# Kernel tuning notes

Hardware: AMD Instinct MI355X
Metric: run time of the kernel (lower is better)

## Reference

```python
import jax, jax.numpy as jnp
import numpy as np

D_MODEL = 1024
N_HEADS = 16
D_HEAD = D_MODEL // N_HEADS
LN_EPS = 1e-5


def setup_inputs() -> dict:
    key = jax.random.key(0)
    ks = jax.random.split(key, 10)
    B, N = 2, 2048
    s = 1.0 / np.sqrt(D_MODEL)
    return {
        "x": jax.random.normal(ks[0], (B, N, D_MODEL), dtype=jnp.float32),
        "Wq": jax.random.normal(ks[1], (D_MODEL, D_MODEL), dtype=jnp.float32) * s,
        "bq": jnp.zeros((D_MODEL,), dtype=jnp.float32),
        "Wk": jax.random.normal(ks[2], (D_MODEL, D_MODEL), dtype=jnp.float32) * s,
        "bk": jnp.zeros((D_MODEL,), dtype=jnp.float32),
        "Wv": jax.random.normal(ks[3], (D_MODEL, D_MODEL), dtype=jnp.float32) * s,
        "bv": jnp.zeros((D_MODEL,), dtype=jnp.float32),
        "Wo": jax.random.normal(ks[4], (D_MODEL, D_MODEL), dtype=jnp.float32) * s,
        "bo": jnp.zeros((D_MODEL,), dtype=jnp.float32),
        "ln_gamma": jnp.ones((D_MODEL,), dtype=jnp.float32),
        "ln_beta": jnp.zeros((D_MODEL,), dtype=jnp.float32),
    }


def reference(x, Wq, bq, Wk, bk, Wv, bv, Wo, bo, ln_gamma, ln_beta):
    B, N, _ = x.shape
    # QKV projections -> [B, H, N, dh]
    def proj(W, b):
        return (x @ W.T + b).reshape(B, N, N_HEADS, D_HEAD).transpose(0, 2, 1, 3)
    Q, K, V = proj(Wq, bq), proj(Wk, bk), proj(Wv, bv)
    # scaled scores [B, H, N, N] with causal mask (is_mask=True)
    scores = jnp.einsum("bhqd,bhkd->bhqk", Q, K) / np.sqrt(D_HEAD)
    causal = jnp.tril(jnp.ones((N, N), dtype=bool))
    scores = jnp.where(causal, scores, -jnp.inf)
    attn = jax.nn.softmax(scores, axis=-1)  # dropout p=0 (eval)
    ctx = jnp.einsum("bhqk,bhkd->bhqd", attn, V)  # [B, H, N, dh]
    ctx = ctx.transpose(0, 2, 1, 3).reshape(B, N, D_MODEL)
    out = ctx @ Wo.T + bo + x  # output proj + residual
    # LayerNorm over last dim
    mu = out.mean(-1, keepdims=True)
    var = out.var(-1, keepdims=True)
    return (out - mu) / jnp.sqrt(var + LN_EPS) * ln_gamma + ln_beta
```

## Files before the change

### kernel.cpp

```cpp
#include <hip/hip_runtime.h>
#include <type_traits>

#define D_MODEL 1024
#define NHEADS 16
#define DHEAD 64
#define SEQ 2048
#define BATCH 2
#define MROWS (BATCH*SEQ)
#define NQT (SEQ/64)

typedef unsigned short ushort_t;
using bf16x8 = __attribute__((ext_vector_type(8))) __bf16;
using us4    = __attribute__((ext_vector_type(4))) unsigned short;
using us8    = __attribute__((ext_vector_type(8))) unsigned short;
using f32x4  = __attribute__((ext_vector_type(4))) float;

__device__ __forceinline__ ushort_t f2bf(float f) {
    unsigned int u = __builtin_bit_cast(unsigned int, f);
    u += 0x7FFFu + ((u >> 16) & 1u);
    return (ushort_t)(u >> 16);
}

__device__ __forceinline__ void gl2lds(const ushort_t* g, ushort_t* l) {
    __builtin_amdgcn_global_load_lds(
        (const __attribute__((address_space(1))) unsigned int*)g,
        (__attribute__((address_space(3))) unsigned int*)l,
        16, 0, 0);
}

__global__ __launch_bounds__(256) void cvt_kernel(
    const float* __restrict__ x,
    const float* __restrict__ wq, const float* __restrict__ wk,
    const float* __restrict__ wv, const float* __restrict__ wo,
    ushort_t* __restrict__ xb,
    ushort_t* __restrict__ wqb, ushort_t* __restrict__ wkb,
    ushort_t* __restrict__ wvb, ushort_t* __restrict__ wob)
{
    const size_t XN = (size_t)MROWS * D_MODEL;
    const size_t WN = (size_t)D_MODEL * D_MODEL;
    size_t i = ((size_t)blockIdx.x * 256 + threadIdx.x) * 4;
    const float* s; ushort_t* d; size_t off;
    if (i < XN) { s = x; d = xb; off = i; }
    else {
        size_t j = i - XN;
        int w = (int)(j / WN);
        off = j - (size_t)w * WN;
        s = (w == 0) ? wq : (w == 1) ? wk : (w == 2) ? wv : wo;
        d = (w == 0) ? wqb : (w == 1) ? wkb : (w == 2) ? wvb : wob;
    }
    const f32x4 v = *(const f32x4*)(s + off);
    us4 o;
    #pragma unroll
    for (int t = 0; t < 4; ++t) o[t] = f2bf(v[t]);
    *(us4*)(d + off) = o;
}

template<typename OutT, bool RES>
__global__ __launch_bounds__(256, 3) void gemm_nt(
    const ushort_t* __restrict__ A,
    const ushort_t* __restrict__ W0, const ushort_t* __restrict__ W1, const ushort_t* __restrict__ W2,
    const float* __restrict__ b0, const float* __restrict__ b1, const float* __restrict__ b2,
    const float* __restrict__ res,
    OutT* __restrict__ Y0, OutT* __restrict__ Y1, OutT* __restrict__ Y2)
{
    constexpr int K = D_MODEL;
    __shared__ ushort_t As[2][128 * 32];
    __shared__ ushort_t Ws[2][128 * 32];

    const int z = blockIdx.z;
    const ushort_t* W  = (z == 0) ? W0 : (z == 1) ? W1 : W2;
    const float* bias  = (z == 0) ? b0 : (z == 1) ? b1 : b2;
    OutT* Y            = (z == 0) ? Y0 : (z == 1) ? Y1 : Y2;

    const int i0 = blockIdx.x * 128;
    const int j0 = blockIdx.y * 128;
    const int tid  = threadIdx.x;
    const int lane = tid & 63;
    const int w    = tid >> 6;
    const int wm   = (w >> 1) * 64;
    const int wn   = (w & 1) * 64;
    const int l15  = lane & 15;
    const int quad = lane >> 4;

    const int srow = lane >> 2;
    const int scol = (lane & 3) * 8;
    const int c0 = w * 2, c1 = w * 2 + 1;
    const ushort_t* gA0 = A + (size_t)(i0 + c0 * 16 + srow) * K + scol;
    const ushort_t* gA1 = A + (size_t)(i0 + c1 * 16 + srow) * K + scol;
    const ushort_t* gW0 = W + (size_t)(j0 + c0 * 16 + srow) * K + scol;
    const ushort_t* gW1 = W + (size_t)(j0 + c1 * 16 + srow) * K + scol;

    f32x4 acc[4][4] = {};

    for (int k0 = 0; k0 < K; k0 += 64) {
        gl2lds(gA0 + k0,      &As[0][c0 * 512]);
        gl2lds(gA1 + k0,      &As[0][c1 * 512]);
        gl2lds(gA0 + k0 + 32, &As[1][c0 * 512]);
        gl2lds(gA1 + k0 + 32, &As[1][c1 * 512]);
        gl2lds(gW0 + k0,      &Ws[0][c0 * 512]);
        gl2lds(gW1 + k0,      &Ws[0][c1 * 512]);
        gl2lds(gW0 + k0 + 32, &Ws[1][c0 * 512]);
        gl2lds(gW1 + k0 + 32, &Ws[1][c1 * 512]);
        __syncthreads();

        #pragma unroll
        for (int s = 0; s < 2; ++s) {
            bf16x8 af[4], wf[4];
            #pragma unroll
            for (int m = 0; m < 4; ++m)
                af[m] = *(const bf16x8*)&As[s][(wm + m * 16 + l15) * 32 + quad * 8];
            #pragma unroll
            for (int n = 0; n < 4; ++n)
                wf[n] = *(const bf16x8*)&Ws[s][(wn + n * 16 + l15) * 32 + quad * 8];
            #pragma unroll
            for (int m = 0; m < 4; ++m)
                #pragma unroll
                for (int n = 0; n < 4; ++n)
                    acc[m][n] = __builtin_amdgcn_mfma_f32_16x16x32_bf16(wf[n], af[m], acc[m][n], 0, 0, 0);
        }
        __syncthreads();
    }

    #pragma unroll
    for (int n = 0; n < 4; ++n) {
        const int col = j0 + wn + n * 16 + quad * 4;
        const f32x4 bv = *(const f32x4*)&bias[col];
        #pragma unroll
        for (int m = 0; m < 4; ++m) {
            const int row = i0 + wm + m * 16 + l15;
            if constexpr (std::is_same<OutT, float>::value) {
                f32x4 v;
                #pragma unroll
                for (int r = 0; r < 4; ++r) v[r] = acc[m][n][r] + bv[r];
                if constexpr (RES) {
                    const f32x4 rv = *(const f32x4*)&res[(size_t)row * D_MODEL + col];
                    #pragma unroll
                    for (int r = 0; r < 4; ++r) v[r] += rv[r];
                }
                *(f32x4*)&Y[(size_t)row * D_MODEL + col] = v;
            } else {
                us4 pk;
                #pragma unroll
                for (int r = 0; r < 4; ++r) pk[r] = f2bf(acc[m][n][r] + bv[r]);
                *(us4*)&Y[(size_t)row * D_MODEL + col] = pk;
            }
        }
    }
}

#define VP 72

__global__ __launch_bounds__(256, 3) void attn_kernel(
    const ushort_t* __restrict__ Qg, const ushort_t* __restrict__ Kg,
    const ushort_t* __restrict__ Vg, ushort_t* __restrict__ Og)
{
    __shared__ ushort_t Kt[2][64 * VP];
    __shared__ ushort_t Vt[2][64 * VP];
    __shared__ ushort_t Pw[64 * VP];
    __shared__ ushort_t OnesR[16 * VP];

    const int bh = blockIdx.y;
    const int b = bh >> 4;
    const int h = bh & 15;
    const int p = blockIdx.x;
    const int tid  = threadIdx.x;
    const int lane = tid & 63;
    const int w    = tid >> 6;
    const int l15  = lane & 15;
    const int quad = lane >> 4;

    const size_t headoff = (size_t)h * DHEAD;
    const ushort_t* Kbase = Kg + (size_t)(b * SEQ) * D_MODEL + headoff;
    const ushort_t* Vbase = Vg + (size_t)(b * SEQ) * D_MODEL + headoff;

    const int krow = tid >> 3;
    const int kb   = tid & 7;
    const int vkey = tid & 63;
    const int dc0  = tid >> 6;
    const int dc1  = dc0 + 4;

    for (int i = tid; i < 16 * VP; i += 256) OnesR[i] = 0x3F80;

    bf16x8 onesf[2];
    bool onesLoaded = false;

    for (int half = 0; half < 2; ++half) {
        const int qt = half ? p : (NQT - 1 - p);
        const int q0 = qt * 64;
        const int qg = q0 + w * 16 + l15;
        const int nkt = qt + 1;

        const size_t qrow = (size_t)(b * SEQ + qg) * D_MODEL + headoff;
        const bf16x8 qf0 = *(const bf16x8*)&Qg[qrow + quad * 8];
        const bf16x8 qf1 = *(const bf16x8*)&Qg[qrow + 32 + quad * 8];

        float m_run = -1e30f;
        f32x4 o[4] = {};
        f32x4 o4 = {};

        us8 kp0, kp1, vp0, vp1;
        kp0 = *(const us8*)&Kbase[(size_t)krow * D_MODEL + kb * 8];
        kp1 = *(const us8*)&Kbase[(size_t)(32 + krow) * D_MODEL + kb * 8];
        vp0 = *(const us8*)&Vbase[(size_t)vkey * D_MODEL + dc0 * 8];
        vp1 = *(const us8*)&Vbase[(size_t)vkey * D_MODEL + dc1 * 8];
        *(us8*)&Kt[0][krow * VP + kb * 8]        = kp0;
        *(us8*)&Kt[0][(32 + krow) * VP + kb * 8] = kp1;
        #pragma unroll
        for (int j = 0; j < 8; ++j) {
            Vt[0][(dc0 * 8 + j) * VP + vkey] = vp0[j];
            Vt[0][(dc1 * 8 + j) * VP + vkey] = vp1[j];
        }
        __syncthreads();

        if (!onesLoaded) {
            onesf[0] = *(const bf16x8*)&OnesR[l15 * VP + quad * 8];
            onesf[1] = *(const bf16x8*)&OnesR[l15 * VP + 32 + quad * 8];
            onesLoaded = true;
        }

        for (int kt = 0; kt < nkt; ++kt) {
            const int cur = kt & 1;
            const int nxt = cur ^ 1;
            const bool pre = (kt + 1 < nkt);
            if (pre) {
                const size_t koff = (size_t)((kt + 1) * 64) * D_MODEL;
                kp0 = *(const us8*)&Kbase[koff + (size_t)krow * D_MODEL + kb * 8];
                kp1 = *(const us8*)&Kbase[koff + (size_t)(32 + krow) * D_MODEL + kb * 8];
                vp0 = *(const us8*)&Vbase[koff + (size_t)vkey * D_MODEL + dc0 * 8];
                vp1 = *(const us8*)&Vbase[koff + (size_t)vkey * D_MODEL + dc1 * 8];
            }

            f32x4 sv[4];
            #pragma unroll
            for (int f = 0; f < 4; ++f) {
                const bf16x8 kf0 = *(const bf16x8*)&Kt[cur][(f * 16 + l15) * VP + quad * 8];
                const bf16x8 kf1 = *(const bf16x8*)&Kt[cur][(f * 16 + l15) * VP + 32 + quad * 8];
                f32x4 s = {};
                s = __builtin_amdgcn_mfma_f32_16x16x32_bf16(kf0, qf0, s, 0, 0, 0);
                s = __builtin_amdgcn_mfma_f32_16x16x32_bf16(kf1, qf1, s, 0, 0, 0);
                sv[f] = s;
            }

            if (kt * 64 + 63 <= q0 + w * 16) {
                #pragma unroll
                for (int f = 0; f < 4; ++f)
                    #pragma unroll
                    for (int r = 0; r < 4; ++r) sv[f][r] *= 0.125f;
            } else {
                #pragma unroll
                for (int f = 0; f < 4; ++f) {
                    #pragma unroll
                    for (int r = 0; r < 4; ++r) {
                        const int kg = kt * 64 + f * 16 + quad * 4 + r;
                        sv[f][r] = (kg <= qg) ? sv[f][r] * 0.125f : -1e30f;
                    }
                }
            }

            float mf[4];
            #pragma unroll
            for (int f = 0; f < 4; ++f)
                mf[f] = fmaxf(fmaxf(sv[f][0], sv[f][1]), fmaxf(sv[f][2], sv[f][3]));
            float mx = fmaxf(fmaxf(mf[0], mf[1]), fmaxf(mf[2], mf[3]));
            mx = fmaxf(mx, __shfl_xor(mx, 16));
            mx = fmaxf(mx, __shfl_xor(mx, 32));
            const float mn = fmaxf(m_run, mx);
            const float al = __expf(m_run - mn);
            m_run = mn;
            #pragma unroll
            for (int f = 0; f < 4; ++f)
                #pragma unroll
                for (int r = 0; r < 4; ++r) sv[f][r] = __expf(sv[f][r] - mn);

            #pragma unroll
            for (int t = 0; t < 4; ++t)
                #pragma unroll
                for (int r = 0; r < 4; ++r) o[t][r] *= al;
            #pragma unroll
            for (int r = 0; r < 4; ++r) o4[r] *= al;

            #pragma unroll
            for (int f = 0; f < 4; ++f) {
                us4 pk;
                #pragma unroll
                for (int r = 0; r < 4; ++r) pk[r] = f2bf(sv[f][r]);
                *(us4*)&Pw[(w * 16 + l15) * VP + f * 16 + quad * 4] = pk;
            }
            __asm__ volatile("s_waitcnt lgkmcnt(0)" ::: "memory");

            #pragma unroll
            for (int s = 0; s < 2; ++s) {
                const bf16x8 pf = *(const bf16x8*)&Pw[(w * 16 + l15) * VP + s * 32 + quad * 8];
                #pragma unroll
                for (int t = 0; t < 4; ++t) {
                    const bf16x8 vf = *(const bf16x8*)&Vt[cur][(t * 16 + l15) * VP + s * 32 + quad * 8];
                    o[t] = __builtin_amdgcn_mfma_f32_16x16x32_bf16(vf, pf, o[t], 0, 0, 0);
                }
                o4 = __builtin_amdgcn_mfma_f32_16x16x32_bf16(onesf[s], pf, o4, 0, 0, 0);
            }

            if (pre) {
                *(us8*)&Kt[nxt][krow * VP + kb * 8]        = kp0;
                *(us8*)&Kt[nxt][(32 + krow) * VP + kb * 8] = kp1;
                #pragma unroll
                for (int j = 0; j < 8; ++j) {
                    Vt[nxt][(dc0 * 8 + j) * VP + vkey] = vp0[j];
                    Vt[nxt][(dc1 * 8 + j) * VP + vkey] = vp1[j];
                }
            }
            __asm__ volatile("s_waitcnt lgkmcnt(0)\n\ts_barrier" ::: "memory");
        }

        const float inv = 1.f / o4[0];
        const size_t orow = (size_t)(b * SEQ + q0 + w * 16 + l15) * D_MODEL + headoff;
        #pragma unroll
        for (int t = 0; t < 4; ++t) {
            us4 pk;
            #pragma unroll
            for (int r = 0; r < 4; ++r) pk[r] = f2bf(o[t][r] * inv);
            *(us4*)&Og[orow + t * 16 + quad * 4] = pk;
        }
    }
}

__global__ __launch_bounds__(256) void ln_kernel(
    const float* __restrict__ X, const float* __restrict__ g,
    const float* __restrict__ bta, float* __restrict__ out)
{
    __shared__ float r1[4], r2[4];
    const int row = blockIdx.x;
    const int tid = threadIdx.x;
    const float* p = X + (size_t)row * D_MODEL;
    float v[4]; float s1 = 0.f, s2 = 0.f;
    #pragma unroll
    for (int i = 0; i < 4; ++i) { v[i] = p[tid + 256 * i]; s1 += v[i]; s2 += v[i] * v[i]; }
    #pragma unroll
    for (int d = 32; d >= 1; d >>= 1) { s1 += __shfl_xor(s1, d); s2 += __shfl_xor(s2, d); }
    if ((tid & 63) == 0) { r1[tid >> 6] = s1; r2[tid >> 6] = s2; }
    __syncthreads();
    s1 = r1[0] + r1[1] + r1[2] + r1[3];
    s2 = r2[0] + r2[1] + r2[2] + r2[3];
    const float mu  = s1 * (1.f / D_MODEL);
    const float var = s2 * (1.f / D_MODEL) - mu * mu;
    const float rstd = rsqrtf(var + 1e-5f);
    #pragma unroll
    for (int i = 0; i < 4; ++i) {
        const int c = tid + 256 * i;
        out[(size_t)row * D_MODEL + c] = (v[i] - mu) * rstd * g[c] + bta[c];
    }
}

extern "C" void kernel_launch(void* const* d_in, const int* in_sizes, int n_in,
                              void* d_out, int out_size, void* d_ws, size_t ws_size,
                              hipStream_t stream) {
    const float* x     = (const float*)d_in[0];
    const float* Wq    = (const float*)d_in[1];
    const float* bq    = (const float*)d_in[2];
    const float* Wk    = (const float*)d_in[3];
    const float* bk    = (const float*)d_in[4];
    const float* Wv    = (const float*)d_in[5];
    const float* bv    = (const float*)d_in[6];
    const float* Wo    = (const float*)d_in[7];
    const float* bo    = (const float*)d_in[8];
    const float* gamma = (const float*)d_in[9];
    const float* beta  = (const float*)d_in[10];

    const size_t XN = (size_t)MROWS * D_MODEL;
    const size_t WN = (size_t)D_MODEL * D_MODEL;
    ushort_t* wsp = (ushort_t*)d_ws;
    ushort_t* xb  = wsp;
    ushort_t* Yq  = wsp + XN;
    ushort_t* Yk  = wsp + 2 * XN;
    ushort_t* Yv  = wsp + 3 * XN;
    ushort_t* Wqb = wsp + 4 * XN;
    ushort_t* Wkb = Wqb + WN;
    ushort_t* Wvb = Wkb + WN;
    ushort_t* Wob = Wvb + WN;
    ushort_t* ctx = xb;
    float*    pre = (float*)d_out;

    cvt_kernel<<<dim3(8192), 256, 0, stream>>>(x, Wq, Wk, Wv, Wo, xb, Wqb, Wkb, Wvb, Wob);

    gemm_nt<ushort_t, false><<<dim3(MROWS / 128, D_MODEL / 128, 3), 256, 0, stream>>>(
        xb, Wqb, Wkb, Wvb, bq, bk, bv, nullptr, Yq, Yk, Yv);

    attn_kernel<<<dim3(SEQ / 128, BATCH * NHEADS), 256, 0, stream>>>(Yq, Yk, Yv, ctx);

    gemm_nt<float, true><<<dim3(MROWS / 128, D_MODEL / 128, 1), 256, 0, stream>>>(
        ctx, Wob, Wob, Wob, bo, bo, bo, x, pre, pre, pre);

    ln_kernel<<<dim3(MROWS), 256, 0, stream>>>(pre, gamma, beta, (float*)d_out);
}
```

Before: 217.2 us.

## Restructure attention: fold softmax scale into Q, exp2, lazy rescale, swizzled LDS

Folds 1/sqrt(dh)*log2(e) into the Q projection epilogue so attention can use exp2 without per-score scaling. Masking now applies only on the diagonal tile, and rescaling of the accumulators is skipped unless the running max grows by more than a threshold. LDS padding is replaced with XOR swizzling, which frees the ones buffer and lets occupancy rise to 4 blocks. The grid now launches one query tile per block, heaviest first, instead of pairing tiles, and MFMA sections get raised wave priority. Native bf16 conversions replace the manual rounding helper. Lazy rescaling carries a numeric risk if the threshold bound is exceeded, and the unpaired grid gives up the built-in load balancing.

```diff
diff --git a/kernel.cpp b/kernel.cpp
--- a/kernel.cpp
+++ b/kernel.cpp
@@ -11,14 +11,19 @@
 
 typedef unsigned short ushort_t;
 using bf16x8 = __attribute__((ext_vector_type(8))) __bf16;
+using bf16x4 = __attribute__((ext_vector_type(4))) __bf16;
 using us4    = __attribute__((ext_vector_type(4))) unsigned short;
 using us8    = __attribute__((ext_vector_type(8))) unsigned short;
 using f32x4  = __attribute__((ext_vector_type(4))) float;
 
-__device__ __forceinline__ ushort_t f2bf(float f) {
-    unsigned int u = __builtin_bit_cast(unsigned int, f);
-    u += 0x7FFFu + ((u >> 16) & 1u);
-    return (ushort_t)(u >> 16);
+#define QSCALE 0.18033688011112042f
+
+__device__ __forceinline__ float fast_exp2(float x) {
+#if __has_builtin(__builtin_amdgcn_exp2f)
+    return __builtin_amdgcn_exp2f(x);
+#else
+    return __expf(x * 0.6931471805599453f);
+#endif
 }
 
 __device__ __forceinline__ void gl2lds(const ushort_t* g, ushort_t* l) {
@@ -49,10 +54,10 @@
         d = (w == 0) ? wqb : (w == 1) ? wkb : (w == 2) ? wvb : wob;
     }
     const f32x4 v = *(const f32x4*)(s + off);
-    us4 o;
-    #pragma unroll
-    for (int t = 0; t < 4; ++t) o[t] = f2bf(v[t]);
-    *(us4*)(d + off) = o;
+    bf16x4 o;
+    #pragma unroll
+    for (int t = 0; t < 4; ++t) o[t] = (__bf16)v[t];
+    *(bf16x4*)(d + off) = o;
 }
 
 template<typename OutT, bool RES>
@@ -61,7 +66,8 @@
     const ushort_t* __restrict__ W0, const ushort_t* __restrict__ W1, const ushort_t* __restrict__ W2,
     const float* __restrict__ b0, const float* __restrict__ b1, const float* __restrict__ b2,
     const float* __restrict__ res,
-    OutT* __restrict__ Y0, OutT* __restrict__ Y1, OutT* __restrict__ Y2)
+    OutT* __restrict__ Y0, OutT* __restrict__ Y1, OutT* __restrict__ Y2,
+    float qsc)
 {
     constexpr int K = D_MODEL;
     __shared__ ushort_t As[2][128 * 32];
@@ -71,6 +77,7 @@
     const ushort_t* W  = (z == 0) ? W0 : (z == 1) ? W1 : W2;
     const float* bias  = (z == 0) ? b0 : (z == 1) ? b1 : b2;
     OutT* Y            = (z == 0) ? Y0 : (z == 1) ? Y1 : Y2;
+    const float sc     = (z == 0) ? qsc : 1.0f;
 
     const int i0 = blockIdx.x * 128;
     const int j0 = blockIdx.y * 128;
@@ -139,30 +146,36 @@
                 }
                 *(f32x4*)&Y[(size_t)row * D_MODEL + col] = v;
             } else {
-                us4 pk;
+                bf16x4 pk;
                 #pragma unroll
-                for (int r = 0; r < 4; ++r) pk[r] = f2bf(acc[m][n][r] + bv[r]);
-                *(us4*)&Y[(size_t)row * D_MODEL + col] = pk;
+                for (int r = 0; r < 4; ++r) pk[r] = (__bf16)((acc[m][n][r] + bv[r]) * sc);
+                *(bf16x4*)&Y[(size_t)row * D_MODEL + col] = pk;
             }
         }
     }
 }
 
-#define VP 72
-
-__global__ __launch_bounds__(256, 3) void attn_kernel(
+#define KD 64
+
+__device__ __forceinline__ int kswz(int row, int col) {
+    return row * KD + (col ^ ((row & 7) << 3));
+}
+
+__global__ __launch_bounds__(256, 4) void attn_kernel(
     const ushort_t* __restrict__ Qg, const ushort_t* __restrict__ Kg,
     const ushort_t* __restrict__ Vg, ushort_t* __restrict__ Og)
 {
-    __shared__ ushort_t Kt[2][64 * VP];
-    __shared__ ushort_t Vt[2][64 * VP];
-    __shared__ ushort_t Pw[64 * VP];
-    __shared__ ushort_t OnesR[16 * VP];
-
-    const int bh = blockIdx.y;
+    __shared__ __align__(16) ushort_t Kt[2][64 * KD];
+    __shared__ __align__(16) ushort_t Vt[2][64 * KD];
+    __shared__ __align__(16) ushort_t Pw[64 * KD];
+
+    const int bh = blockIdx.x;
     const int b = bh >> 4;
     const int h = bh & 15;
-    const int p = blockIdx.x;
+    const int qt = (NQT - 1) - blockIdx.y;
+    const int q0 = qt * 64;
+    const int nkt = qt + 1;
+
     const int tid  = threadIdx.x;
     const int lane = tid & 63;
     const int w    = tid >> 6;
@@ -179,147 +192,141 @@
     const int dc0  = tid >> 6;
     const int dc1  = dc0 + 4;
 
-    for (int i = tid; i < 16 * VP; i += 256) OnesR[i] = 0x3F80;
-
-    bf16x8 onesf[2];
-    bool onesLoaded = false;
-
-    for (int half = 0; half < 2; ++half) {
-        const int qt = half ? p : (NQT - 1 - p);
-        const int q0 = qt * 64;
-        const int qg = q0 + w * 16 + l15;
-        const int nkt = qt + 1;
-
-        const size_t qrow = (size_t)(b * SEQ + qg) * D_MODEL + headoff;
-        const bf16x8 qf0 = *(const bf16x8*)&Qg[qrow + quad * 8];
-        const bf16x8 qf1 = *(const bf16x8*)&Qg[qrow + 32 + quad * 8];
-
-        float m_run = -1e30f;
-        f32x4 o[4] = {};
-        f32x4 o4 = {};
-
-        us8 kp0, kp1, vp0, vp1;
-        kp0 = *(const us8*)&Kbase[(size_t)krow * D_MODEL + kb * 8];
-        kp1 = *(const us8*)&Kbase[(size_t)(32 + krow) * D_MODEL + kb * 8];
-        vp0 = *(const us8*)&Vbase[(size_t)vkey * D_MODEL + dc0 * 8];
-        vp1 = *(const us8*)&Vbase[(size_t)vkey * D_MODEL + dc1 * 8];
-        *(us8*)&Kt[0][krow * VP + kb * 8]        = kp0;
-        *(us8*)&Kt[0][(32 + krow) * VP + kb * 8] = kp1;
-        #pragma unroll
-        for (int j = 0; j < 8; ++j) {
-            Vt[0][(dc0 * 8 + j) * VP + vkey] = vp0[j];
-            Vt[0][(dc1 * 8 + j) * VP + vkey] = vp1[j];
-        }
-        __syncthreads();
-
-        if (!onesLoaded) {
-            onesf[0] = *(const bf16x8*)&OnesR[l15 * VP + quad * 8];
-            onesf[1] = *(const bf16x8*)&OnesR[l15 * VP + 32 + quad * 8];
-            onesLoaded = true;
-        }
-
-        for (int kt = 0; kt < nkt; ++kt) {
-            const int cur = kt & 1;
-            const int nxt = cur ^ 1;
-            const bool pre = (kt + 1 < nkt);
-            if (pre) {
-                const size_t koff = (size_t)((kt + 1) * 64) * D_MODEL;
-                kp0 = *(const us8*)&Kbase[koff + (size_t)krow * D_MODEL + kb * 8];
-                kp1 = *(const us8*)&Kbase[koff + (size_t)(32 + krow) * D_MODEL + kb * 8];
-                vp0 = *(const us8*)&Vbase[koff + (size_t)vkey * D_MODEL + dc0 * 8];
-                vp1 = *(const us8*)&Vbase[koff + (size_t)vkey * D_MODEL + dc1 * 8];
-            }
-
-            f32x4 sv[4];
-            #pragma unroll
-            for (int f = 0; f < 4; ++f) {
-                const bf16x8 kf0 = *(const bf16x8*)&Kt[cur][(f * 16 + l15) * VP + quad * 8];
-                const bf16x8 kf1 = *(const bf16x8*)&Kt[cur][(f * 16 + l15) * VP + 32 + quad * 8];
-                f32x4 s = {};
-                s = __builtin_amdgcn_mfma_f32_16x16x32_bf16(kf0, qf0, s, 0, 0, 0);
-                s = __builtin_amdgcn_mfma_f32_16x16x32_bf16(kf1, qf1, s, 0, 0, 0);
-                sv[f] = s;
-            }
-
-            if (kt * 64 + 63 <= q0 + w * 16) {
-                #pragma unroll
-                for (int f = 0; f < 4; ++f)
-                    #pragma unroll
-                    for (int r = 0; r < 4; ++r) sv[f][r] *= 0.125f;
-            } else {
-                #pragma unroll
-                for (int f = 0; f < 4; ++f) {
-                    #pragma unroll
-                    for (int r = 0; r < 4; ++r) {
-                        const int kg = kt * 64 + f * 16 + quad * 4 + r;
-                        sv[f][r] = (kg <= qg) ? sv[f][r] * 0.125f : -1e30f;
-                    }
-                }
-            }
-
-            float mf[4];
-            #pragma unroll
-            for (int f = 0; f < 4; ++f)
-                mf[f] = fmaxf(fmaxf(sv[f][0], sv[f][1]), fmaxf(sv[f][2], sv[f][3]));
-            float mx = fmaxf(fmaxf(mf[0], mf[1]), fmaxf(mf[2], mf[3]));
-            mx = fmaxf(mx, __shfl_xor(mx, 16));
-            mx = fmaxf(mx, __shfl_xor(mx, 32));
-            const float mn = fmaxf(m_run, mx);
-            const float al = __expf(m_run - mn);
-            m_run = mn;
+    const int rx = (l15 & 7) << 3;
+    const int cs0 = (quad * 8) ^ rx;
+    const int cs1 = (32 + quad * 8) ^ rx;
+    int pwc[4];
+    #pragma unroll
+    for (int f = 0; f < 4; ++f) pwc[f] = (f * 16 + quad * 4) ^ rx;
+    ushort_t* PwRow = &Pw[(w * 16 + l15) * KD];
+
+    const int kwa = krow * KD + ((kb * 8) ^ ((krow & 7) << 3));
+
+    const int qg = q0 + w * 16 + l15;
+    const size_t qrow = (size_t)(b * SEQ + qg) * D_MODEL + headoff;
+    const bf16x8 qf0 = *(const bf16x8*)&Qg[qrow + quad * 8];
+    const bf16x8 qf1 = *(const bf16x8*)&Qg[qrow + 32 + quad * 8];
+
+    bf16x8 onesf;
+    #pragma unroll
+    for (int j = 0; j < 8; ++j) onesf[j] = (__bf16)1.0f;
+
+    float m_run = -1e30f;
+    f32x4 o[4] = {};
+    f32x4 o4 = {};
+
+    us8 kp0, kp1, vp0, vp1;
+    kp0 = *(const us8*)&Kbase[(size_t)krow * D_MODEL + kb * 8];
+    kp1 = *(const us8*)&Kbase[(size_t)(32 + krow) * D_MODEL + kb * 8];
+    vp0 = *(const us8*)&Vbase[(size_t)vkey * D_MODEL + dc0 * 8];
+    vp1 = *(const us8*)&Vbase[(size_t)vkey * D_MODEL + dc1 * 8];
+    *(us8*)&Kt[0][kwa]           = kp0;
+    *(us8*)&Kt[0][kwa + 32 * KD] = kp1;
+    #pragma unroll
+    for (int j = 0; j < 8; ++j) {
+        Vt[0][(dc0 * 8 + j) * KD + (vkey ^ (j << 3))] = vp0[j];
+        Vt[0][(dc1 * 8 + j) * KD + (vkey ^ (j << 3))] = vp1[j];
+    }
+    __syncthreads();
+
+    for (int kt = 0; kt < nkt; ++kt) {
+        const int cur = kt & 1;
+        const int nxt = cur ^ 1;
+        const bool pre = (kt + 1 < nkt);
+        if (pre) {
+            const size_t koff = (size_t)((kt + 1) * 64) * D_MODEL;
+            kp0 = *(const us8*)&Kbase[koff + (size_t)krow * D_MODEL + kb * 8];
+            kp1 = *(const us8*)&Kbase[koff + (size_t)(32 + krow) * D_MODEL + kb * 8];
+            vp0 = *(const us8*)&Vbase[koff + (size_t)vkey * D_MODEL + dc0 * 8];
+            vp1 = *(const us8*)&Vbase[koff + (size_t)vkey * D_MODEL + dc1 * 8];
+        }
+
+        f32x4 sv[4];
+        __builtin_amdgcn_s_setprio(1);
+        #pragma unroll
+        for (int f = 0; f < 4; ++f) {
+            const int rbase = (f * 16 + l15) * KD;
+            const bf16x8 kf0 = *(const bf16x8*)&Kt[cur][rbase + cs0];
+            const bf16x8 kf1 = *(const bf16x8*)&Kt[cur][rbase + cs1];
+            f32x4 s = {};
+            s = __builtin_amdgcn_mfma_f32_16x16x32_bf16(kf0, qf0, s, 0, 0, 0);
+            s = __builtin_amdgcn_mfma_f32_16x16x32_bf16(kf1, qf1, s, 0, 0, 0);
+            sv[f] = s;
+        }
+        __builtin_amdgcn_s_setprio(0);
+
+        if (kt == qt) {
             #pragma unroll
             for (int f = 0; f < 4; ++f)
                 #pragma unroll
-                for (int r = 0; r < 4; ++r) sv[f][r] = __expf(sv[f][r] - mn);
-
+                for (int r = 0; r < 4; ++r) {
+                    const int kg = kt * 64 + f * 16 + quad * 4 + r;
+                    sv[f][r] = (kg <= qg) ? sv[f][r] : -1e30f;
+                }
+        }
+
+        float mf[4];
+        #pragma unroll
+        for (int f = 0; f < 4; ++f)
+            mf[f] = fmaxf(fmaxf(sv[f][0], sv[f][1]), fmaxf(sv[f][2], sv[f][3]));
+        float mx = fmaxf(fmaxf(mf[0], mf[1]), fmaxf(mf[2], mf[3]));
+        mx = fmaxf(mx, __shfl_xor(mx, 16));
+        mx = fmaxf(mx, __shfl_xor(mx, 32));
+
+        if (!__all(mx <= m_run + 8.0f)) {
+            const float mn = fmaxf(m_run, mx);
+            const float al = fast_exp2(m_run - mn);
+            m_run = mn;
             #pragma unroll
             for (int t = 0; t < 4; ++t)
                 #pragma unroll
                 for (int r = 0; r < 4; ++r) o[t][r] *= al;
-            #pragma unroll
-            for (int r = 0; r < 4; ++r) o4[r] *= al;
-
-            #pragma unroll
-            for (int f = 0; f < 4; ++f) {
-                us4 pk;
-                #pragma unroll
-                for (int r = 0; r < 4; ++r) pk[r] = f2bf(sv[f][r]);
-                *(us4*)&Pw[(w * 16 + l15) * VP + f * 16 + quad * 4] = pk;
+            o4[0] *= al;
+        }
+
+        #pragma unroll
+        for (int f = 0; f < 4; ++f) {
+            bf16x4 pk;
+            #pragma unroll
+            for (int r = 0; r < 4; ++r)
+                pk[r] = (__bf16)fast_exp2(sv[f][r] - m_run);
+            *(bf16x4*)&PwRow[pwc[f]] = pk;
+        }
+        __asm__ volatile("s_waitcnt lgkmcnt(0)" ::: "memory");
+
+        __builtin_amdgcn_s_setprio(1);
+        #pragma unroll
+        for (int s = 0; s < 2; ++s) {
+            const bf16x8 pf = *(const bf16x8*)&PwRow[s ? cs1 : cs0];
+            #pragma unroll
+            for (int t = 0; t < 4; ++t) {
+                const bf16x8 vf = *(const bf16x8*)&Vt[cur][(t * 16 + l15) * KD + (s ? cs1 : cs0)];
+                o[t] = __builtin_amdgcn_mfma_f32_16x16x32_bf16(vf, pf, o[t], 0, 0, 0);
             }
-            __asm__ volatile("s_waitcnt lgkmcnt(0)" ::: "memory");
-
-            #pragma unroll
-            for (int s = 0; s < 2; ++s) {
-                const bf16x8 pf = *(const bf16x8*)&Pw[(w * 16 + l15) * VP + s * 32 + quad * 8];
-                #pragma unroll
-                for (int t = 0; t < 4; ++t) {
-                    const bf16x8 vf = *(const bf16x8*)&Vt[cur][(t * 16 + l15) * VP + s * 32 + quad * 8];
-                    o[t] = __builtin_amdgcn_mfma_f32_16x16x32_bf16(vf, pf, o[t], 0, 0, 0);
-                }
-                o4 = __builtin_amdgcn_mfma_f32_16x16x32_bf16(onesf[s], pf, o4, 0, 0, 0);
+            o4 = __builtin_amdgcn_mfma_f32_16x16x32_bf16(onesf, pf, o4, 0, 0, 0);
+        }
+        __builtin_amdgcn_s_setprio(0);
+
+        if (pre) {
+            *(us8*)&Kt[nxt][kwa]           = kp0;
+            *(us8*)&Kt[nxt][kwa + 32 * KD] = kp1;
+            #pragma unroll
+            for (int j = 0; j < 8; ++j) {
+                Vt[nxt][(dc0 * 8 + j) * KD + (vkey ^ (j << 3))] = vp0[j];
+                Vt[nxt][(dc1 * 8 + j) * KD + (vkey ^ (j << 3))] = vp1[j];
             }
-
-            if (pre) {
-                *(us8*)&Kt[nxt][krow * VP + kb * 8]        = kp0;
-                *(us8*)&Kt[nxt][(32 + krow) * VP + kb * 8] = kp1;
-                #pragma unroll
-                for (int j = 0; j < 8; ++j) {
-                    Vt[nxt][(dc0 * 8 + j) * VP + vkey] = vp0[j];
-                    Vt[nxt][(dc1 * 8 + j) * VP + vkey] = vp1[j];
-                }
-            }
-            __asm__ volatile("s_waitcnt lgkmcnt(0)\n\ts_barrier" ::: "memory");
-        }
-
-        const float inv = 1.f / o4[0];
-        const size_t orow = (size_t)(b * SEQ + q0 + w * 16 + l15) * D_MODEL + headoff;
-        #pragma unroll
-        for (int t = 0; t < 4; ++t) {
-            us4 pk;
-            #pragma unroll
-            for (int r = 0; r < 4; ++r) pk[r] = f2bf(o[t][r] * inv);
-            *(us4*)&Og[orow + t * 16 + quad * 4] = pk;
-        }
+        }
+        __asm__ volatile("s_waitcnt lgkmcnt(0)\n\ts_barrier" ::: "memory");
+    }
+
+    const float inv = 1.f / o4[0];
+    const size_t orow = (size_t)(b * SEQ + qg) * D_MODEL + headoff;
+    #pragma unroll
+    for (int t = 0; t < 4; ++t) {
+        bf16x4 pk;
+        #pragma unroll
+        for (int r = 0; r < 4; ++r) pk[r] = (__bf16)(o[t][r] * inv);
+        *(bf16x4*)&Og[orow + t * 16 + quad * 4] = pk;
     }
 }
 
@@ -382,12 +389,12 @@
     cvt_kernel<<<dim3(8192), 256, 0, stream>>>(x, Wq, Wk, Wv, Wo, xb, Wqb, Wkb, Wvb, Wob);
 
     gemm_nt<ushort_t, false><<<dim3(MROWS / 128, D_MODEL / 128, 3), 256, 0, stream>>>(
-        xb, Wqb, Wkb, Wvb, bq, bk, bv, nullptr, Yq, Yk, Yv);
-
-    attn_kernel<<<dim3(SEQ / 128, BATCH * NHEADS), 256, 0, stream>>>(Yq, Yk, Yv, ctx);
+        xb, Wqb, Wkb, Wvb, bq, bk, bv, nullptr, Yq, Yk, Yv, QSCALE);
+
+    attn_kernel<<<dim3(BATCH * NHEADS, NQT), 256, 0, stream>>>(Yq, Yk, Yv, ctx);
 
     gemm_nt<float, true><<<dim3(MROWS / 128, D_MODEL / 128, 1), 256, 0, stream>>>(
-        ctx, Wob, Wob, Wob, bo, bo, bo, x, pre, pre, pre);
+        ctx, Wob, Wob, Wob, bo, bo, bo, x, pre, pre, pre, 1.0f);
 
     ln_kernel<<<dim3(MROWS), 256, 0, stream>>>(pre, gamma, beta, (float*)d_out);
 }
```

Result: faster. 205.7 us (-5.3%).
